# Performance work log

Measured on AMD Instinct MI355X. Metric: run time of the kernel, lower is better.

Reference implementation:

```python
import jax, jax.numpy as jnp
import numpy as np

N = 100000   # nodes
E = 1600000  # edges (avg degree 16)
IN, H, OUT = 64, 128, 1


def setup_inputs() -> dict:
    key = jax.random.key(0)
    ks = jax.random.split(key, 12)
    s = 0.05
    return {
        "x": jax.random.normal(ks[0], (N, IN), jnp.float32),
        "edge_index": jax.random.randint(ks[1], (2, E), 0, N, dtype=jnp.int64),
        "Wl1": jax.random.normal(ks[2], (IN, H), jnp.float32) * s,
        "Wr1": jax.random.normal(ks[3], (IN, H), jnp.float32) * s,
        "b1": jnp.zeros((H,), jnp.float32),
        "ln_g": jnp.ones((H,), jnp.float32),
        "ln_b": jnp.zeros((H,), jnp.float32),
        "Wres": jax.random.normal(ks[4], (IN, H), jnp.float32) * s,
        "bres": jnp.zeros((H,), jnp.float32),
        "Wl2": jax.random.normal(ks[5], (H, H), jnp.float32) * s,
        "Wr2": jax.random.normal(ks[6], (H, H), jnp.float32) * s,
        "b2": jnp.zeros((H,), jnp.float32),
        "Wl3": jax.random.normal(ks[7], (H, H), jnp.float32) * s,
        "Wr3": jax.random.normal(ks[8], (H, H), jnp.float32) * s,
        "b3": jnp.zeros((H,), jnp.float32),
        "Wl4": jax.random.normal(ks[9], (H, OUT), jnp.float32) * s,
        "Wr4": jax.random.normal(ks[10], (H, OUT), jnp.float32) * s,
        "b4": jnp.zeros((OUT,), jnp.float32),
    }


def _sage(h, src, dst, deg_inv, Wl, Wr, b):
    # PyG SAGEConv, aggr='mean': lin_l(mean_{j in N(i)} h_j) + lin_r(h_i)
    agg = jax.ops.segment_sum(h[src], dst, num_segments=N) * deg_inv[:, None]
    return agg @ Wl + h @ Wr + b


def _layernorm(h, g, b, eps=1e-5):
    mu = jnp.mean(h, axis=-1, keepdims=True)
    var = jnp.mean((h - mu) ** 2, axis=-1, keepdims=True)
    return (h - mu) * jax.lax.rsqrt(var + eps) * g + b


def reference(x, edge_index, Wl1, Wr1, b1, ln_g, ln_b, Wres, bres,
              Wl2, Wr2, b2, Wl3, Wr3, b3, Wl4, Wr4, b4):
    src, dst = edge_index[0], edge_index[1]
    deg = jax.ops.segment_sum(jnp.ones((E,), jnp.float32), dst, num_segments=N)
    deg_inv = 1.0 / jnp.maximum(deg, 1.0)

    h = jax.nn.relu(_layernorm(_sage(x, src, dst, deg_inv, Wl1, Wr1, b1), ln_g, ln_b))
    h = h + x @ Wres + bres              # residual (in_channel != hidden_channel)
    h = jax.nn.relu(_sage(h, src, dst, deg_inv, Wl2, Wr2, b2))   # dropout: eval no-op
    h = jax.nn.relu(_sage(h, src, dst, deg_inv, Wl3, Wr3, b3))
    out = _sage(h, src, dst, deg_inv, Wl4, Wr4, b4)
    return out.squeeze(-1)
```

## Files before the change

kernel.cpp:

```cpp
#include <hip/hip_runtime.h>
#include <hip/hip_bf16.h>

#define N_NODES 100000
#define N_EDGES 1600000

#define NBKT 782
#define SCAT_BLOCKS 240
#define BKT_CHUNK 6667

#define SORT_BLOCKS 40
#define SORT_CHUNK 2500
#define BH2_N (NBKT * SCAT_BLOCKS)
#define BHB ((BH2_N + 1023) / 1024)
#define XBF_BLOCKS 6250

#define NSTRIPS 6250
#define GEMM_BLOCKS 782

typedef __attribute__((ext_vector_type(8))) short short8v;
typedef __attribute__((ext_vector_type(4))) float float4v;

__device__ __forceinline__ unsigned short f2bf(float f) {
    unsigned int u = __float_as_uint(f);
    u = (u + 0x7FFFu + ((u >> 16) & 1u)) >> 16;
    return (unsigned short)u;
}
__device__ __forceinline__ float bf2f(unsigned short b) {
    return __uint_as_float((unsigned int)b << 16);
}

typedef __attribute__((address_space(1))) const unsigned int gld_g_t;
typedef __attribute__((address_space(3))) unsigned int gld_l_t;
__device__ __forceinline__ void gld_lds16(const void* g, void* l) {
    __builtin_amdgcn_global_load_lds((gld_g_t*)g, (gld_l_t*)l, 16, 0, 0);
}

#define SWZ128(row, ksh) ((row) * 128 + ((ksh) ^ (((row) & 7) << 3)))
#define SWZ256(row, ksh) ((row) * 256 + ((ksh) ^ (((row) & 7) << 3)))

__global__ __launch_bounds__(256) void hist_xbf_kernel(const int* __restrict__ ei, int* __restrict__ bh2,
                                                       const float* __restrict__ x, unsigned short* __restrict__ xcat) {
    __shared__ int h[NBKT];
    int tid = threadIdx.x;
    if (blockIdx.x < SCAT_BLOCKS) {
        for (int i = tid; i < NBKT; i += 256) h[i] = 0;
        __syncthreads();
        int start = blockIdx.x * BKT_CHUNK;
        int end = start + BKT_CHUNK; if (end > N_EDGES) end = N_EDGES;
        for (int i = start + tid; i < end; i += 256) {
            int d = ei[N_EDGES + i];
            atomicAdd(&h[d >> 7], 1);
        }
        __syncthreads();
        for (int i = tid; i < NBKT; i += 256) bh2[i * SCAT_BLOCKS + blockIdx.x] = h[i];
    } else {
        int idx = (blockIdx.x - SCAT_BLOCKS) * 256 + tid;
        if (idx < N_NODES * 16) {
            int node = idx >> 4;
            int f0 = (idx & 15) * 4;
            float4 v = *(const float4*)(x + (size_t)idx * 4);
            ushort4 o;
            o.x = f2bf(v.x); o.y = f2bf(v.y); o.z = f2bf(v.z); o.w = f2bf(v.w);
            *(ushort4*)(xcat + (size_t)node * 128 + f0) = o;
        }
    }
}

__global__ __launch_bounds__(256) void gscan_a_kernel(const int* __restrict__ in, int* __restrict__ bsum, int n) {
    __shared__ int lds[256];
    int tid = threadIdx.x;
    int base = blockIdx.x * 1024 + tid * 4;
    int s = 0;
    #pragma unroll
    for (int i = 0; i < 4; i++) s += (base + i < n) ? in[base + i] : 0;
    lds[tid] = s;
    __syncthreads();
    for (int off = 128; off; off >>= 1) {
        if (tid < off) lds[tid] += lds[tid + off];
        __syncthreads();
    }
    if (tid == 0) bsum[blockIdx.x] = lds[0];
}

__global__ __launch_bounds__(256) void gscan_c_kernel(int* __restrict__ data, const int* __restrict__ bsum,
                                                      int nb, int n) {
    __shared__ int sb[256];
    __shared__ int lds[256];
    int tid = threadIdx.x;
    sb[tid] = (tid < nb) ? bsum[tid] : 0;
    __syncthreads();
    for (int off = 1; off < 256; off <<= 1) {
        int y = 0;
        if (tid >= off) y = sb[tid - off];
        __syncthreads();
        if (tid >= off) sb[tid] += y;
        __syncthreads();
    }
    int blockbase = (blockIdx.x == 0) ? 0 : sb[blockIdx.x - 1];

    int base = blockIdx.x * 1024 + tid * 4;
    int v[4];
    int s = 0;
    #pragma unroll
    for (int i = 0; i < 4; i++) {
        v[i] = (base + i < n) ? data[base + i] : 0;
        s += v[i];
    }
    lds[tid] = s;
    __syncthreads();
    for (int off = 1; off < 256; off <<= 1) {
        int y = 0;
        if (tid >= off) y = lds[tid - off];
        __syncthreads();
        if (tid >= off) lds[tid] += y;
        __syncthreads();
    }
    int run = blockbase + lds[tid] - s;
    #pragma unroll
    for (int i = 0; i < 4; i++) {
        if (base + i < n) data[base + i] = run;
        run += v[i];
    }
}

__global__ __launch_bounds__(256) void bkt_scatter2_kernel(const int* __restrict__ ei, const int* __restrict__ bh2,
                                                           int* __restrict__ packed) {
    __shared__ int h[NBKT];
    __shared__ int base[NBKT];
    int tid = threadIdx.x;
    for (int i = tid; i < NBKT; i += 256) { h[i] = 0; base[i] = bh2[i * SCAT_BLOCKS + blockIdx.x]; }
    __syncthreads();
    int start = blockIdx.x * BKT_CHUNK;
    int end = start + BKT_CHUNK; if (end > N_EDGES) end = N_EDGES;
    for (int i = start + tid; i < end; i += 256) {
        int s = ei[i];
        int d = ei[N_EDGES + i];
        int b = d >> 7;
        int pos = base[b] + atomicAdd(&h[b], 1);
        packed[pos] = (s << 7) | (d & 127);
    }
}

__global__ __launch_bounds__(256) void bkt_build_kernel(const int* __restrict__ packed, const int* __restrict__ bh2,
                                                        int* __restrict__ deg, int* __restrict__ row_ptr,
                                                        int* __restrict__ col) {
    __shared__ int c[128];
    __shared__ int rp[128];
    int tid = threadIdx.x;
    int s0 = bh2[blockIdx.x * SCAT_BLOCKS];
    int s1 = (blockIdx.x + 1 < NBKT) ? bh2[(blockIdx.x + 1) * SCAT_BLOCKS] : N_EDGES;
    if (tid < 128) c[tid] = 0;
    __syncthreads();
    for (int i = s0 + tid; i < s1; i += 256) atomicAdd(&c[packed[i] & 127], 1);
    __syncthreads();
    if (tid < 128) rp[tid] = c[tid];
    __syncthreads();
    for (int off = 1; off < 128; off <<= 1) {
        int y = 0;
        if (tid >= off && tid < 128) y = rp[tid - off];
        __syncthreads();
        if (tid >= off && tid < 128) rp[tid] += y;
        __syncthreads();
    }
    int node = blockIdx.x * 128 + tid;
    if (tid < 128) {
        rp[tid] = s0 + rp[tid] - c[tid];
        if (node < N_NODES) {
            deg[node] = c[tid];
            row_ptr[node] = rp[tid];
        }
        c[tid] = 0;
    }
    if (blockIdx.x == 0 && tid == 0) row_ptr[N_NODES] = N_EDGES;
    __syncthreads();
    for (int i = s0 + tid; i < s1; i += 256) {
        int p = packed[i];
        int dl = p & 127;
        int pos = rp[dl] + atomicAdd(&c[dl], 1);
        col[pos] = p >> 7;
    }
}

__global__ __launch_bounds__(256) void dsort_hist_kernel(const int* __restrict__ deg, int* __restrict__ bh) {
    __shared__ int h[64];
    int tid = threadIdx.x;
    if (tid < 64) h[tid] = 0;
    __syncthreads();
    int start = blockIdx.x * SORT_CHUNK;
    int end = start + SORT_CHUNK; if (end > N_NODES) end = N_NODES;
    for (int i = start + tid; i < end; i += 256) atomicAdd(&h[min(deg[i], 63)], 1);
    __syncthreads();
    if (tid < 64) bh[tid * SORT_BLOCKS + blockIdx.x] = h[tid];
}

__global__ __launch_bounds__(256) void dsort_scat_kernel(const int* __restrict__ deg, const int* __restrict__ bh,
                                                         int* __restrict__ ord) {
    __shared__ int sbh[64 * SORT_BLOCKS];
    __shared__ int ps[256];
    __shared__ int h[64];
    int tid = threadIdx.x;
    int v[10];
    int s = 0;
    #pragma unroll
    for (int k = 0; k < 10; k++) { v[k] = bh[tid * 10 + k]; s += v[k]; }
    ps[tid] = s;
    if (tid < 64) h[tid] = 0;
    __syncthreads();
    for (int off = 1; off < 256; off <<= 1) {
        int y = 0;
        if (tid >= off) y = ps[tid - off];
        __syncthreads();
        if (tid >= off) ps[tid] += y;
        __syncthreads();
    }
    int run = ps[tid] - s;
    #pragma unroll
    for (int k = 0; k < 10; k++) { sbh[tid * 10 + k] = run; run += v[k]; }
    __syncthreads();
    int start = blockIdx.x * SORT_CHUNK;
    int end = start + SORT_CHUNK; if (end > N_NODES) end = N_NODES;
    for (int i = start + tid; i < end; i += 256) {
        int b = min(deg[i], 63);
        int pos = sbh[b * SORT_BLOCKS + blockIdx.x] + atomicAdd(&h[b], 1);
        ord[pos] = i;
    }
}

#define ACC4(u) { a0 += bf2f(u.x); a1 += bf2f(u.y); a2 += bf2f(u.z); a3 += bf2f(u.w); }

__global__ __launch_bounds__(256) void agg64_kernel(unsigned short* __restrict__ xcat,
                                                    const int* __restrict__ row_ptr, const int* __restrict__ col,
                                                    const int* __restrict__ ord) {
    int tid = threadIdx.x;
    int slot = blockIdx.x * 16 + (tid >> 4);
    if (slot >= N_NODES) return;
    int i = ord[slot];
    int f0 = (tid & 15) * 4;
    int s = row_ptr[i], e = row_ptr[i + 1];
    float a0 = 0.f, a1 = 0.f, a2 = 0.f, a3 = 0.f;
    int t = s;
    while (t + 7 < e) {
        int j0 = col[t], j1 = col[t + 1], j2 = col[t + 2], j3 = col[t + 3];
        int j4 = col[t + 4], j5 = col[t + 5], j6 = col[t + 6], j7 = col[t + 7];
        ushort4 u0 = *(const ushort4*)(xcat + (size_t)j0 * 128 + f0);
        ushort4 u1 = *(const ushort4*)(xcat + (size_t)j1 * 128 + f0);
        ushort4 u2 = *(const ushort4*)(xcat + (size_t)j2 * 128 + f0);
        ushort4 u3 = *(const ushort4*)(xcat + (size_t)j3 * 128 + f0);
        ushort4 u4 = *(const ushort4*)(xcat + (size_t)j4 * 128 + f0);
        ushort4 u5 = *(const ushort4*)(xcat + (size_t)j5 * 128 + f0);
        ushort4 u6 = *(const ushort4*)(xcat + (size_t)j6 * 128 + f0);
        ushort4 u7 = *(const ushort4*)(xcat + (size_t)j7 * 128 + f0);
        ACC4(u0) ACC4(u1) ACC4(u2) ACC4(u3) ACC4(u4) ACC4(u5) ACC4(u6) ACC4(u7)
        t += 8;
    }
    if (t + 3 < e) {
        int j0 = col[t], j1 = col[t + 1], j2 = col[t + 2], j3 = col[t + 3];
        ushort4 u0 = *(const ushort4*)(xcat + (size_t)j0 * 128 + f0);
        ushort4 u1 = *(const ushort4*)(xcat + (size_t)j1 * 128 + f0);
        ushort4 u2 = *(const ushort4*)(xcat + (size_t)j2 * 128 + f0);
        ushort4 u3 = *(const ushort4*)(xcat + (size_t)j3 * 128 + f0);
        ACC4(u0) ACC4(u1) ACC4(u2) ACC4(u3)
        t += 4;
    }
    if (t + 1 < e) {
        int j0 = col[t], j1 = col[t + 1];
        ushort4 u0 = *(const ushort4*)(xcat + (size_t)j0 * 128 + f0);
        ushort4 u1 = *(const ushort4*)(xcat + (size_t)j1 * 128 + f0);
        ACC4(u0) ACC4(u1)
        t += 2;
    }
    if (t < e) {
        ushort4 u0 = *(const ushort4*)(xcat + (size_t)col[t] * 128 + f0);
        ACC4(u0)
    }
    float di = 1.0f / fmaxf((float)(e - s), 1.0f);
    ushort4 o;
    o.x = f2bf(a0 * di); o.y = f2bf(a1 * di); o.z = f2bf(a2 * di); o.w = f2bf(a3 * di);
    *(ushort4*)(xcat + (size_t)i * 128 + 64 + f0) = o;
}

__global__ __launch_bounds__(256) void agg128_kernel(unsigned short* __restrict__ hcat,
                                                     const int* __restrict__ row_ptr, const int* __restrict__ col,
                                                     const int* __restrict__ ord) {
    int tid = threadIdx.x;
    int slot = blockIdx.x * 8 + (tid >> 5);
    if (slot >= N_NODES) return;
    int i = ord[slot];
    int f0 = (tid & 31) * 4;
    int s = row_ptr[i], e = row_ptr[i + 1];
    float a0 = 0.f, a1 = 0.f, a2 = 0.f, a3 = 0.f;
    int t = s;
    while (t + 7 < e) {
        int j0 = col[t], j1 = col[t + 1], j2 = col[t + 2], j3 = col[t + 3];
        int j4 = col[t + 4], j5 = col[t + 5], j6 = col[t + 6], j7 = col[t + 7];
        ushort4 u0 = *(const ushort4*)(hcat + (size_t)j0 * 256 + f0);
        ushort4 u1 = *(const ushort4*)(hcat + (size_t)j1 * 256 + f0);
        ushort4 u2 = *(const ushort4*)(hcat + (size_t)j2 * 256 + f0);
        ushort4 u3 = *(const ushort4*)(hcat + (size_t)j3 * 256 + f0);
        ushort4 u4 = *(const ushort4*)(hcat + (size_t)j4 * 256 + f0);
        ushort4 u5 = *(const ushort4*)(hcat + (size_t)j5 * 256 + f0);
        ushort4 u6 = *(const ushort4*)(hcat + (size_t)j6 * 256 + f0);
        ushort4 u7 = *(const ushort4*)(hcat + (size_t)j7 * 256 + f0);
        ACC4(u0) ACC4(u1) ACC4(u2) ACC4(u3) ACC4(u4) ACC4(u5) ACC4(u6) ACC4(u7)
        t += 8;
    }
    if (t + 3 < e) {
        int j0 = col[t], j1 = col[t + 1], j2 = col[t + 2], j3 = col[t + 3];
        ushort4 u0 = *(const ushort4*)(hcat + (size_t)j0 * 256 + f0);
        ushort4 u1 = *(const ushort4*)(hcat + (size_t)j1 * 256 + f0);
        ushort4 u2 = *(const ushort4*)(hcat + (size_t)j2 * 256 + f0);
        ushort4 u3 = *(const ushort4*)(hcat + (size_t)j3 * 256 + f0);
        ACC4(u0) ACC4(u1) ACC4(u2) ACC4(u3)
        t += 4;
    }
    if (t + 1 < e) {
        int j0 = col[t], j1 = col[t + 1];
        ushort4 u0 = *(const ushort4*)(hcat + (size_t)j0 * 256 + f0);
        ushort4 u1 = *(const ushort4*)(hcat + (size_t)j1 * 256 + f0);
        ACC4(u0) ACC4(u1)
        t += 2;
    }
    if (t < e) {
        ushort4 u0 = *(const ushort4*)(hcat + (size_t)col[t] * 256 + f0);
        ACC4(u0)
    }
    float di = 1.0f / fmaxf((float)(e - s), 1.0f);
    ushort4 o;
    o.x = f2bf(a0 * di); o.y = f2bf(a1 * di); o.z = f2bf(a2 * di); o.w = f2bf(a3 * di);
    *(ushort4*)(hcat + (size_t)i * 256 + 128 + f0) = o;
}

__global__ __launch_bounds__(256) void wprep_all_kernel(const float* __restrict__ Wr1, const float* __restrict__ Wl1,
                                                        const float* __restrict__ Wres,
                                                        const float* __restrict__ Wl2, const float* __restrict__ Wr2,
                                                        const float* __restrict__ Wl3, const float* __restrict__ Wr3,
                                                        unsigned short* __restrict__ Bt1,
                                                        unsigned short* __restrict__ Bt2,
                                                        unsigned short* __restrict__ Bt3) {
    int idx = blockIdx.x * 256 + threadIdx.x;
    int seg = idx >> 15;
    int loc = idx & 32767;
    if (seg == 0) {
        int n = loc >> 7;
        int k = loc & 127;
        float v;
        if (n < 128) v = (k < 64) ? Wr1[k * 128 + n] : Wl1[(k - 64) * 128 + n];
        else         v = (k < 64) ? Wres[k * 128 + (n - 128)] : 0.f;
        Bt1[loc] = f2bf(v);
    } else if (seg == 1) {
        int n = loc >> 8;
        int k = loc & 255;
        float v = (k < 128) ? Wr2[k * 128 + n] : Wl2[(k - 128) * 128 + n];
        Bt2[loc] = f2bf(v);
    } else if (seg == 2) {
        int n = loc >> 8;
        int k = loc & 255;
        float v = (k < 128) ? Wr3[k * 128 + n] : Wl3[(k - 128) * 128 + n];
        Bt3[loc] = f2bf(v);
    }
}

__global__ __launch_bounds__(512) void mgemm1_ln_kernel(const unsigned short* __restrict__ A,
                                                        const unsigned short* __restrict__ Bt,
                                                        const float* __restrict__ b1, const float* __restrict__ ln_g,
                                                        const float* __restrict__ ln_b, const float* __restrict__ bres,
                                                        unsigned short* __restrict__ hcat) {
    __shared__ unsigned short Bs[32768];
    int tid = threadIdx.x;
    int wave = tid >> 6, lane = tid & 63;
    int lm = lane & 15, lk = (lane >> 4) * 8;

    #pragma unroll
    for (int rnd = 0; rnd < 8; rnd++) {
        int Lb = rnd * 8192 + tid * 16;
        int row = Lb >> 8;
        int sb = (Lb & 255) ^ ((row & 7) << 4);
        gld_lds16(Bt + (size_t)row * 128 + (sb >> 1), &Bs[Lb >> 1]);
    }
    __syncthreads();

    int strip = blockIdx.x * 8 + wave;
    if (strip >= NSTRIPS) return;
    int m0 = strip * 16;

    float4v accT[8], accR[8];
    #pragma unroll
    for (int j = 0; j < 8; j++) { accT[j] = (float4v)0.f; accR[j] = (float4v)0.f; }

    const unsigned short* arow = A + (size_t)(m0 + lm) * 128 + lk;
    #pragma unroll
    for (int k0 = 0; k0 < 128; k0 += 32) {
        short8v af = *(const short8v*)(arow + k0);
        short8v bf[8];
        #pragma unroll
        for (int j = 0; j < 8; j++)
            bf[j] = *(const short8v*)&Bs[SWZ128(j * 16 + lm, k0 + lk)];
        #pragma unroll
        for (int j = 0; j < 8; j++)
            accT[j] = __builtin_amdgcn_mfma_f32_16x16x32_bf16(af, bf[j], accT[j], 0, 0, 0);
        if (k0 < 64) {
            short8v bg[8];
            #pragma unroll
            for (int j = 0; j < 8; j++)
                bg[j] = *(const short8v*)&Bs[SWZ128(128 + j * 16 + lm, k0 + lk)];
            #pragma unroll
            for (int j = 0; j < 8; j++)
                accR[j] = __builtin_amdgcn_mfma_f32_16x16x32_bf16(af, bg[j], accR[j], 0, 0, 0);
        }
    }

    float b1v[8], gv[8], bbv[8], brv[8];
    #pragma unroll
    for (int j = 0; j < 8; j++) {
        int cc = j * 16 + lm;
        b1v[j] = b1[cc]; gv[j] = ln_g[cc]; bbv[j] = ln_b[cc]; brv[j] = bres[cc];
    }
    int q4 = lane >> 4;
    #pragma unroll
    for (int r = 0; r < 4; r++) {
        float sp = 0.f, sq = 0.f;
        #pragma unroll
        for (int j = 0; j < 8; j++) {
            float tv = accT[j][r] + b1v[j];
            sp += tv; sq += tv * tv;
        }
        #pragma unroll
        for (int off = 1; off < 16; off <<= 1) {
            sp += __shfl_xor(sp, off);
            sq += __shfl_xor(sq, off);
        }
        float mu = sp * (1.f / 128.f);
        float var = sq * (1.f / 128.f) - mu * mu;
        float rstd = rsqrtf(var + 1e-5f);
        int gm = m0 + q4 * 4 + r;
        #pragma unroll
        for (int j = 0; j < 8; j++) {
            float tv = accT[j][r] + b1v[j];
            float y = fmaxf((tv - mu) * rstd * gv[j] + bbv[j], 0.f) + accR[j][r] + brv[j];
            hcat[(size_t)gm * 256 + j * 16 + lm] = f2bf(y);
        }
    }
}

__global__ __launch_bounds__(512) void mgemm_kernel(const unsigned short* __restrict__ A,
                                                    const unsigned short* __restrict__ Bt,
                                                    const float* __restrict__ bias,
                                                    unsigned short* __restrict__ C) {
    __shared__ unsigned short Bs[32768];
    int tid = threadIdx.x;
    int wave = tid >> 6, lane = tid & 63;
    int lm = lane & 15, lk = (lane >> 4) * 8;

    #pragma unroll
    for (int rnd = 0; rnd < 8; rnd++) {
        int Lb = rnd * 8192 + tid * 16;
        int row = Lb >> 9;
        int sb = (Lb & 511) ^ ((row & 7) << 4);
        gld_lds16(Bt + ((size_t)row << 8) + (sb >> 1), &Bs[Lb >> 1]);
    }
    __syncthreads();

    int strip = blockIdx.x * 8 + wave;
    if (strip >= NSTRIPS) return;
    int m0 = strip * 16;

    float4v acc[8];
    #pragma unroll
    for (int j = 0; j < 8; j++) acc[j] = (float4v)0.f;

    const unsigned short* arow = A + (size_t)(m0 + lm) * 256 + lk;
    #pragma unroll
    for (int k0 = 0; k0 < 256; k0 += 32) {
        short8v af = *(const short8v*)(arow + k0);
        short8v bf[8];
        #pragma unroll
        for (int j = 0; j < 8; j++)
            bf[j] = *(const short8v*)&Bs[SWZ256(j * 16 + lm, k0 + lk)];
        #pragma unroll
        for (int j = 0; j < 8; j++)
            acc[j] = __builtin_amdgcn_mfma_f32_16x16x32_bf16(af, bf[j], acc[j], 0, 0, 0);
    }

    int q4 = lane >> 4;
    #pragma unroll
    for (int j = 0; j < 8; j++) {
        int cc = j * 16 + lm;
        float bv = bias[cc];
        #pragma unroll
        for (int r = 0; r < 4; r++) {
            int m = m0 + q4 * 4 + r;
            C[(size_t)m * 256 + cc] = f2bf(fmaxf(acc[j][r] + bv, 0.f));
        }
    }
}

__global__ __launch_bounds__(512) void mgemm_pq_kernel(const unsigned short* __restrict__ A,
                                                       const unsigned short* __restrict__ Bt,
                                                       const float* __restrict__ bias,
                                                       const float* __restrict__ Wl4, const float* __restrict__ Wr4,
                                                       const float* __restrict__ b4,
                                                       float* __restrict__ p, float* __restrict__ q) {
    __shared__ unsigned short Bs[32768];
    int tid = threadIdx.x;
    int wave = tid >> 6, lane = tid & 63;
    int lm = lane & 15, lk = (lane >> 4) * 8;

    #pragma unroll
    for (int rnd = 0; rnd < 8; rnd++) {
        int Lb = rnd * 8192 + tid * 16;
        int row = Lb >> 9;
        int sb = (Lb & 511) ^ ((row & 7) << 4);
        gld_lds16(Bt + ((size_t)row << 8) + (sb >> 1), &Bs[Lb >> 1]);
    }
    __syncthreads();

    int strip = blockIdx.x * 8 + wave;
    if (strip >= NSTRIPS) return;
    int m0 = strip * 16;

    float4v acc[8];
    #pragma unroll
    for (int j = 0; j < 8; j++) acc[j] = (float4v)0.f;

    const unsigned short* arow = A + (size_t)(m0 + lm) * 256 + lk;
    #pragma unroll
    for (int k0 = 0; k0 < 256; k0 += 32) {
        short8v af = *(const short8v*)(arow + k0);
        short8v bf[8];
        #pragma unroll
        for (int j = 0; j < 8; j++)
            bf[j] = *(const short8v*)&Bs[SWZ256(j * 16 + lm, k0 + lk)];
        #pragma unroll
        for (int j = 0; j < 8; j++)
            acc[j] = __builtin_amdgcn_mfma_f32_16x16x32_bf16(af, bf[j], acc[j], 0, 0, 0);
    }

    float b3v[8], wlv[8], wrv[8];
    #pragma unroll
    for (int j = 0; j < 8; j++) {
        int cc = j * 16 + lm;
        b3v[j] = bias[cc]; wlv[j] = Wl4[cc]; wrv[j] = Wr4[cc];
    }
    float b4v = b4[0];
    int q4 = lane >> 4;
    #pragma unroll
    for (int r = 0; r < 4; r++) {
        float pp = 0.f, qq = 0.f;
        #pragma unroll
        for (int j = 0; j < 8; j++) {
            float hv = fmaxf(acc[j][r] + b3v[j], 0.f);
            pp += hv * wlv[j]; qq += hv * wrv[j];
        }
        #pragma unroll
        for (int off = 1; off < 16; off <<= 1) {
            pp += __shfl_xor(pp, off);
            qq += __shfl_xor(qq, off);
        }
        if (lm == 0) {
            int m = m0 + q4 * 4 + r;
            p[m] = pp;
            q[m] = qq + b4v;
        }
    }
}

__global__ __launch_bounds__(256) void final_kernel(const float* __restrict__ p, const float* __restrict__ q,
                                                    const int* __restrict__ row_ptr, const int* __restrict__ col,
                                                    float* __restrict__ out) {
    int i = blockIdx.x * 256 + threadIdx.x;
    if (i >= N_NODES) return;
    int s = row_ptr[i], e = row_ptr[i + 1];
    float acc = 0.f;
    int t = s;
    for (; t + 3 < e; t += 4)
        acc += p[col[t]] + p[col[t + 1]] + p[col[t + 2]] + p[col[t + 3]];
    for (; t < e; t++) acc += p[col[t]];
    float di = 1.0f / fmaxf((float)(e - s), 1.0f);
    out[i] = acc * di + q[i];
}


extern "C" void kernel_launch(void* const* d_in, const int* in_sizes, int n_in,
                              void* d_out, int out_size, void* d_ws, size_t ws_size,
                              hipStream_t stream) {
    const float* x    = (const float*)d_in[0];
    const int*   ei   = (const int*)d_in[1];
    const float* Wl1  = (const float*)d_in[2];
    const float* Wr1  = (const float*)d_in[3];
    const float* b1   = (const float*)d_in[4];
    const float* ln_g = (const float*)d_in[5];
    const float* ln_b = (const float*)d_in[6];
    const float* Wres = (const float*)d_in[7];
    const float* bres = (const float*)d_in[8];
    const float* Wl2  = (const float*)d_in[9];
    const float* Wr2  = (const float*)d_in[10];
    const float* b2   = (const float*)d_in[11];
    const float* Wl3  = (const float*)d_in[12];
    const float* Wr3  = (const float*)d_in[13];
    const float* b3   = (const float*)d_in[14];
    const float* Wl4  = (const float*)d_in[15];
    const float* Wr4  = (const float*)d_in[16];
    const float* b4   = (const float*)d_in[17];
    float* out = (float*)d_out;

    char* w = (char*)d_ws;
    size_t off = 0;
    auto alloc = [&](size_t bytes) -> void* {
        off = (off + 255) & ~(size_t)255;
        void* pp = w + off;
        off += bytes;
        return pp;
    };

    int*   deg        = (int*)alloc(N_NODES * 4);
    int*   row_ptr    = (int*)alloc((N_NODES + 1) * 4);
    int*   bsum       = (int*)alloc(1024);
    int*   col        = (int*)alloc(N_EDGES * 4);
    int*   bh2        = (int*)alloc(BH2_N * 4);
    int*   bh         = (int*)alloc(64 * SORT_BLOCKS * 4);
    int*   ord        = (int*)alloc(N_NODES * 4);
    unsigned short* Bt1  = (unsigned short*)alloc(256 * 128 * 2);
    unsigned short* Bt2  = (unsigned short*)alloc(128 * 256 * 2);
    unsigned short* Bt3  = (unsigned short*)alloc(128 * 256 * 2);
    unsigned short* xcat = (unsigned short*)alloc((size_t)N_NODES * 128 * 2);
    unsigned short* hcat = (unsigned short*)alloc((size_t)N_NODES * 256 * 2);
    int*   packed  = (int*)alloc((size_t)N_EDGES * 4);
    float* p       = (float*)alloc(N_NODES * 4);
    float* q       = (float*)alloc(N_NODES * 4);
    (void)ws_size; (void)n_in; (void)in_sizes; (void)out_size;

    const int NB = (N_NODES + 255) / 256;

    wprep_all_kernel<<<384, 256, 0, stream>>>(Wr1, Wl1, Wres, Wl2, Wr2, Wl3, Wr3, Bt1, Bt2, Bt3);

    hist_xbf_kernel<<<SCAT_BLOCKS + XBF_BLOCKS, 256, 0, stream>>>(ei, bh2, x, xcat);
    gscan_a_kernel<<<BHB, 256, 0, stream>>>(bh2, bsum, BH2_N);
    gscan_c_kernel<<<BHB, 256, 0, stream>>>(bh2, bsum, BHB, BH2_N);
    bkt_scatter2_kernel<<<SCAT_BLOCKS, 256, 0, stream>>>(ei, bh2, packed);
    bkt_build_kernel<<<NBKT, 256, 0, stream>>>(packed, bh2, deg, row_ptr, col);
    dsort_hist_kernel<<<SORT_BLOCKS, 256, 0, stream>>>(deg, bh);
    dsort_scat_kernel<<<SORT_BLOCKS, 256, 0, stream>>>(deg, bh, ord);

    agg64_kernel<<<(N_NODES + 15) / 16, 256, 0, stream>>>(xcat, row_ptr, col, ord);
    mgemm1_ln_kernel<<<GEMM_BLOCKS, 512, 0, stream>>>(xcat, Bt1, b1, ln_g, ln_b, bres, hcat);

    agg128_kernel<<<(N_NODES + 7) / 8, 256, 0, stream>>>(hcat, row_ptr, col, ord);
    mgemm_kernel<<<GEMM_BLOCKS, 512, 0, stream>>>(hcat, Bt2, b2, hcat);

    agg128_kernel<<<(N_NODES + 7) / 8, 256, 0, stream>>>(hcat, row_ptr, col, ord);
    mgemm_pq_kernel<<<GEMM_BLOCKS, 512, 0, stream>>>(hcat, Bt3, b3, Wl4, Wr4, b4, p, q);

    final_kernel<<<NB, 256, 0, stream>>>(p, q, row_ptr, col, out);
}
```

Before: 372.9 us.

## Split concatenated feature buffers into separate source and aggregate arrays

Concatenated [self | aggregated] bf16 rows are replaced by separate dense source and aggregate arrays. Neighbour gathers then read from a compact table with half the row stride, which shrinks the gathered working set and should improve cache reuse. The GEMMs now read their A operand from two pointers, choosing one per k-step. It also reverses the degree-sort order so high-degree nodes are scheduled first, and unrolls the final scalar gather by 8; the cost is slightly more pointer arithmetic in the GEMM A loads.

```diff
diff --git a/kernel.cpp b/kernel.cpp
--- a/kernel.cpp
+++ b/kernel.cpp
@@ -39,7 +39,7 @@
 #define SWZ256(row, ksh) ((row) * 256 + ((ksh) ^ (((row) & 7) << 3)))
 
 __global__ __launch_bounds__(256) void hist_xbf_kernel(const int* __restrict__ ei, int* __restrict__ bh2,
-                                                       const float* __restrict__ x, unsigned short* __restrict__ xcat) {
+                                                       const float* __restrict__ x, unsigned short* __restrict__ xsrc) {
     __shared__ int h[NBKT];
     int tid = threadIdx.x;
     if (blockIdx.x < SCAT_BLOCKS) {
@@ -61,7 +61,7 @@
             float4 v = *(const float4*)(x + (size_t)idx * 4);
             ushort4 o;
             o.x = f2bf(v.x); o.y = f2bf(v.y); o.z = f2bf(v.z); o.w = f2bf(v.w);
-            *(ushort4*)(xcat + (size_t)node * 128 + f0) = o;
+            *(ushort4*)(xsrc + (size_t)node * 64 + f0) = o;
         }
     }
 }
@@ -188,7 +188,7 @@
     __syncthreads();
     int start = blockIdx.x * SORT_CHUNK;
     int end = start + SORT_CHUNK; if (end > N_NODES) end = N_NODES;
-    for (int i = start + tid; i < end; i += 256) atomicAdd(&h[min(deg[i], 63)], 1);
+    for (int i = start + tid; i < end; i += 256) atomicAdd(&h[63 - min(deg[i], 63)], 1);
     __syncthreads();
     if (tid < 64) bh[tid * SORT_BLOCKS + blockIdx.x] = h[tid];
 }
@@ -220,7 +220,7 @@
     int start = blockIdx.x * SORT_CHUNK;
     int end = start + SORT_CHUNK; if (end > N_NODES) end = N_NODES;
     for (int i = start + tid; i < end; i += 256) {
-        int b = min(deg[i], 63);
+        int b = 63 - min(deg[i], 63);
         int pos = sbh[b * SORT_BLOCKS + blockIdx.x] + atomicAdd(&h[b], 1);
         ord[pos] = i;
     }
@@ -228,7 +228,8 @@
 
 #define ACC4(u) { a0 += bf2f(u.x); a1 += bf2f(u.y); a2 += bf2f(u.z); a3 += bf2f(u.w); }
 
-__global__ __launch_bounds__(256) void agg64_kernel(unsigned short* __restrict__ xcat,
+__global__ __launch_bounds__(256) void agg64_kernel(const unsigned short* __restrict__ xsrc,
+                                                    unsigned short* __restrict__ aggx,
                                                     const int* __restrict__ row_ptr, const int* __restrict__ col,
                                                     const int* __restrict__ ord) {
     int tid = threadIdx.x;
@@ -242,44 +243,45 @@
     while (t + 7 < e) {
         int j0 = col[t], j1 = col[t + 1], j2 = col[t + 2], j3 = col[t + 3];
         int j4 = col[t + 4], j5 = col[t + 5], j6 = col[t + 6], j7 = col[t + 7];
-        ushort4 u0 = *(const ushort4*)(xcat + (size_t)j0 * 128 + f0);
-        ushort4 u1 = *(const ushort4*)(xcat + (size_t)j1 * 128 + f0);
-        ushort4 u2 = *(const ushort4*)(xcat + (size_t)j2 * 128 + f0);
-        ushort4 u3 = *(const ushort4*)(xcat + (size_t)j3 * 128 + f0);
-        ushort4 u4 = *(const ushort4*)(xcat + (size_t)j4 * 128 + f0);
-        ushort4 u5 = *(const ushort4*)(xcat + (size_t)j5 * 128 + f0);
-        ushort4 u6 = *(const ushort4*)(xcat + (size_t)j6 * 128 + f0);
-        ushort4 u7 = *(const ushort4*)(xcat + (size_t)j7 * 128 + f0);
+        ushort4 u0 = *(const ushort4*)(xsrc + (size_t)j0 * 64 + f0);
+        ushort4 u1 = *(const ushort4*)(xsrc + (size_t)j1 * 64 + f0);
+        ushort4 u2 = *(const ushort4*)(xsrc + (size_t)j2 * 64 + f0);
+        ushort4 u3 = *(const ushort4*)(xsrc + (size_t)j3 * 64 + f0);
+        ushort4 u4 = *(const ushort4*)(xsrc + (size_t)j4 * 64 + f0);
+        ushort4 u5 = *(const ushort4*)(xsrc + (size_t)j5 * 64 + f0);
+        ushort4 u6 = *(const ushort4*)(xsrc + (size_t)j6 * 64 + f0);
+        ushort4 u7 = *(const ushort4*)(xsrc + (size_t)j7 * 64 + f0);
         ACC4(u0) ACC4(u1) ACC4(u2) ACC4(u3) ACC4(u4) ACC4(u5) ACC4(u6) ACC4(u7)
         t += 8;
     }
     if (t + 3 < e) {
         int j0 = col[t], j1 = col[t + 1], j2 = col[t + 2], j3 = col[t + 3];
-        ushort4 u0 = *(const ushort4*)(xcat + (size_t)j0 * 128 + f0);
-        ushort4 u1 = *(const ushort4*)(xcat + (size_t)j1 * 128 + f0);
-        ushort4 u2 = *(const ushort4*)(xcat + (size_t)j2 * 128 + f0);
-        ushort4 u3 = *(const ushort4*)(xcat + (size_t)j3 * 128 + f0);
+        ushort4 u0 = *(const ushort4*)(xsrc + (size_t)j0 * 64 + f0);
+        ushort4 u1 = *(const ushort4*)(xsrc + (size_t)j1 * 64 + f0);
+        ushort4 u2 = *(const ushort4*)(xsrc + (size_t)j2 * 64 + f0);
+        ushort4 u3 = *(const ushort4*)(xsrc + (size_t)j3 * 64 + f0);
         ACC4(u0) ACC4(u1) ACC4(u2) ACC4(u3)
         t += 4;
     }
     if (t + 1 < e) {
         int j0 = col[t], j1 = col[t + 1];
-        ushort4 u0 = *(const ushort4*)(xcat + (size_t)j0 * 128 + f0);
-        ushort4 u1 = *(const ushort4*)(xcat + (size_t)j1 * 128 + f0);
+        ushort4 u0 = *(const ushort4*)(xsrc + (size_t)j0 * 64 + f0);
+        ushort4 u1 = *(const ushort4*)(xsrc + (size_t)j1 * 64 + f0);
         ACC4(u0) ACC4(u1)
         t += 2;
     }
     if (t < e) {
-        ushort4 u0 = *(const ushort4*)(xcat + (size_t)col[t] * 128 + f0);
+        ushort4 u0 = *(const ushort4*)(xsrc + (size_t)col[t] * 64 + f0);
         ACC4(u0)
     }
     float di = 1.0f / fmaxf((float)(e - s), 1.0f);
     ushort4 o;
     o.x = f2bf(a0 * di); o.y = f2bf(a1 * di); o.z = f2bf(a2 * di); o.w = f2bf(a3 * di);
-    *(ushort4*)(xcat + (size_t)i * 128 + 64 + f0) = o;
-}
-
-__global__ __launch_bounds__(256) void agg128_kernel(unsigned short* __restrict__ hcat,
+    *(ushort4*)(aggx + (size_t)i * 64 + f0) = o;
+}
+
+__global__ __launch_bounds__(256) void agg128_kernel(const unsigned short* __restrict__ hsrc,
+                                                     unsigned short* __restrict__ aggh,
                                                      const int* __restrict__ row_ptr, const int* __restrict__ col,
                                                      const int* __restrict__ ord) {
     int tid = threadIdx.x;
@@ -293,41 +295,41 @@
     while (t + 7 < e) {
         int j0 = col[t], j1 = col[t + 1], j2 = col[t + 2], j3 = col[t + 3];
         int j4 = col[t + 4], j5 = col[t + 5], j6 = col[t + 6], j7 = col[t + 7];
-        ushort4 u0 = *(const ushort4*)(hcat + (size_t)j0 * 256 + f0);
-        ushort4 u1 = *(const ushort4*)(hcat + (size_t)j1 * 256 + f0);
-        ushort4 u2 = *(const ushort4*)(hcat + (size_t)j2 * 256 + f0);
-        ushort4 u3 = *(const ushort4*)(hcat + (size_t)j3 * 256 + f0);
-        ushort4 u4 = *(const ushort4*)(hcat + (size_t)j4 * 256 + f0);
-        ushort4 u5 = *(const ushort4*)(hcat + (size_t)j5 * 256 + f0);
-        ushort4 u6 = *(const ushort4*)(hcat + (size_t)j6 * 256 + f0);
-        ushort4 u7 = *(const ushort4*)(hcat + (size_t)j7 * 256 + f0);
+        ushort4 u0 = *(const ushort4*)(hsrc + (size_t)j0 * 128 + f0);
+        ushort4 u1 = *(const ushort4*)(hsrc + (size_t)j1 * 128 + f0);
+        ushort4 u2 = *(const ushort4*)(hsrc + (size_t)j2 * 128 + f0);
+        ushort4 u3 = *(const ushort4*)(hsrc + (size_t)j3 * 128 + f0);
+        ushort4 u4 = *(const ushort4*)(hsrc + (size_t)j4 * 128 + f0);
+        ushort4 u5 = *(const ushort4*)(hsrc + (size_t)j5 * 128 + f0);
+        ushort4 u6 = *(const ushort4*)(hsrc + (size_t)j6 * 128 + f0);
+        ushort4 u7 = *(const ushort4*)(hsrc + (size_t)j7 * 128 + f0);
         ACC4(u0) ACC4(u1) ACC4(u2) ACC4(u3) ACC4(u4) ACC4(u5) ACC4(u6) ACC4(u7)
         t += 8;
     }
     if (t + 3 < e) {
         int j0 = col[t], j1 = col[t + 1], j2 = col[t + 2], j3 = col[t + 3];
-        ushort4 u0 = *(const ushort4*)(hcat + (size_t)j0 * 256 + f0);
-        ushort4 u1 = *(const ushort4*)(hcat + (size_t)j1 * 256 + f0);
-        ushort4 u2 = *(const ushort4*)(hcat + (size_t)j2 * 256 + f0);
-        ushort4 u3 = *(const ushort4*)(hcat + (size_t)j3 * 256 + f0);
+        ushort4 u0 = *(const ushort4*)(hsrc + (size_t)j0 * 128 + f0);
+        ushort4 u1 = *(const ushort4*)(hsrc + (size_t)j1 * 128 + f0);
+        ushort4 u2 = *(const ushort4*)(hsrc + (size_t)j2 * 128 + f0);
+        ushort4 u3 = *(const ushort4*)(hsrc + (size_t)j3 * 128 + f0);
         ACC4(u0) ACC4(u1) ACC4(u2) ACC4(u3)
         t += 4;
     }
     if (t + 1 < e) {
         int j0 = col[t], j1 = col[t + 1];
-        ushort4 u0 = *(const ushort4*)(hcat + (size_t)j0 * 256 + f0);
-        ushort4 u1 = *(const ushort4*)(hcat + (size_t)j1 * 256 + f0);
+        ushort4 u0 = *(const ushort4*)(hsrc + (size_t)j0 * 128 + f0);
+        ushort4 u1 = *(const ushort4*)(hsrc + (size_t)j1 * 128 + f0);
         ACC4(u0) ACC4(u1)
         t += 2;
     }
     if (t < e) {
-        ushort4 u0 = *(const ushort4*)(hcat + (size_t)col[t] * 256 + f0);
+        ushort4 u0 = *(const ushort4*)(hsrc + (size_t)col[t] * 128 + f0);
         ACC4(u0)
     }
     float di = 1.0f / fmaxf((float)(e - s), 1.0f);
     ushort4 o;
     o.x = f2bf(a0 * di); o.y = f2bf(a1 * di); o.z = f2bf(a2 * di); o.w = f2bf(a3 * di);
-    *(ushort4*)(hcat + (size_t)i * 256 + 128 + f0) = o;
+    *(ushort4*)(aggh + (size_t)i * 128 + f0) = o;
 }
 
 __global__ __launch_bounds__(256) void wprep_all_kernel(const float* __restrict__ Wr1, const float* __restrict__ Wl1,
@@ -360,11 +362,12 @@
     }
 }
 
-__global__ __launch_bounds__(512) void mgemm1_ln_kernel(const unsigned short* __restrict__ A,
+__global__ __launch_bounds__(512) void mgemm1_ln_kernel(const unsigned short* __restrict__ Ax,
+                                                        const unsigned short* __restrict__ Aa,
                                                         const unsigned short* __restrict__ Bt,
                                                         const float* __restrict__ b1, const float* __restrict__ ln_g,
                                                         const float* __restrict__ ln_b, const float* __restrict__ bres,
-                                                        unsigned short* __restrict__ hcat) {
+                                                        unsigned short* __restrict__ hsrc) {
     __shared__ unsigned short Bs[32768];
     int tid = threadIdx.x;
     int wave = tid >> 6, lane = tid & 63;
@@ -387,10 +390,11 @@
     #pragma unroll
     for (int j = 0; j < 8; j++) { accT[j] = (float4v)0.f; accR[j] = (float4v)0.f; }
 
-    const unsigned short* arow = A + (size_t)(m0 + lm) * 128 + lk;
+    const unsigned short* arx = Ax + (size_t)(m0 + lm) * 64 + lk;
+    const unsigned short* ara = Aa + (size_t)(m0 + lm) * 64 + lk;
     #pragma unroll
     for (int k0 = 0; k0 < 128; k0 += 32) {
-        short8v af = *(const short8v*)(arow + k0);
+        short8v af = (k0 < 64) ? *(const short8v*)(arx + k0) : *(const short8v*)(ara + (k0 - 64));
         short8v bf[8];
         #pragma unroll
         for (int j = 0; j < 8; j++)
@@ -437,12 +441,13 @@
         for (int j = 0; j < 8; j++) {
             float tv = accT[j][r] + b1v[j];
             float y = fmaxf((tv - mu) * rstd * gv[j] + bbv[j], 0.f) + accR[j][r] + brv[j];
-            hcat[(size_t)gm * 256 + j * 16 + lm] = f2bf(y);
-        }
-    }
-}
-
-__global__ __launch_bounds__(512) void mgemm_kernel(const unsigned short* __restrict__ A,
+            hsrc[(size_t)gm * 128 + j * 16 + lm] = f2bf(y);
+        }
+    }
+}
+
+__global__ __launch_bounds__(512) void mgemm_kernel(const unsigned short* __restrict__ Ah,
+                                                    const unsigned short* __restrict__ Aa,
                                                     const unsigned short* __restrict__ Bt,
                                                     const float* __restrict__ bias,
                                                     unsigned short* __restrict__ C) {
@@ -468,10 +473,11 @@
     #pragma unroll
     for (int j = 0; j < 8; j++) acc[j] = (float4v)0.f;
 
-    const unsigned short* arow = A + (size_t)(m0 + lm) * 256 + lk;
+    const unsigned short* arh = Ah + (size_t)(m0 + lm) * 128 + lk;
+    const unsigned short* ara = Aa + (size_t)(m0 + lm) * 128 + lk;
     #pragma unroll
     for (int k0 = 0; k0 < 256; k0 += 32) {
-        short8v af = *(const short8v*)(arow + k0);
+        short8v af = (k0 < 128) ? *(const short8v*)(arh + k0) : *(const short8v*)(ara + (k0 - 128));
         short8v bf[8];
         #pragma unroll
         for (int j = 0; j < 8; j++)
@@ -489,12 +495,13 @@
         #pragma unroll
         for (int r = 0; r < 4; r++) {
             int m = m0 + q4 * 4 + r;
-            C[(size_t)m * 256 + cc] = f2bf(fmaxf(acc[j][r] + bv, 0.f));
-        }
-    }
-}
-
-__global__ __launch_bounds__(512) void mgemm_pq_kernel(const unsigned short* __restrict__ A,
+            C[(size_t)m * 128 + cc] = f2bf(fmaxf(acc[j][r] + bv, 0.f));
+        }
+    }
+}
+
+__global__ __launch_bounds__(512) void mgemm_pq_kernel(const unsigned short* __restrict__ Ah,
+                                                       const unsigned short* __restrict__ Aa,
                                                        const unsigned short* __restrict__ Bt,
                                                        const float* __restrict__ bias,
                                                        const float* __restrict__ Wl4, const float* __restrict__ Wr4,
@@ -522,10 +529,11 @@
     #pragma unroll
     for (int j = 0; j < 8; j++) acc[j] = (float4v)0.f;
 
-    const unsigned short* arow = A + (size_t)(m0 + lm) * 256 + lk;
+    const unsigned short* arh = Ah + (size_t)(m0 + lm) * 128 + lk;
+    const unsigned short* ara = Aa + (size_t)(m0 + lm) * 128 + lk;
     #pragma unroll
     for (int k0 = 0; k0 < 256; k0 += 32) {
-        short8v af = *(const short8v*)(arow + k0);
+        short8v af = (k0 < 128) ? *(const short8v*)(arh + k0) : *(const short8v*)(ara + (k0 - 128));
         short8v bf[8];
         #pragma unroll
         for (int j = 0; j < 8; j++)
@@ -572,8 +580,9 @@
     int s = row_ptr[i], e = row_ptr[i + 1];
     float acc = 0.f;
     int t = s;
-    for (; t + 3 < e; t += 4)
-        acc += p[col[t]] + p[col[t + 1]] + p[col[t + 2]] + p[col[t + 3]];
+    for (; t + 7 < e; t += 8)
+        acc += p[col[t]] + p[col[t + 1]] + p[col[t + 2]] + p[col[t + 3]]
+             + p[col[t + 4]] + p[col[t + 5]] + p[col[t + 6]] + p[col[t + 7]];
     for (; t < e; t++) acc += p[col[t]];
     float di = 1.0f / fmaxf((float)(e - s), 1.0f);
     out[i] = acc * di + q[i];
@@ -622,8 +631,10 @@
     unsigned short* Bt1  = (unsigned short*)alloc(256 * 128 * 2);
     unsigned short* Bt2  = (unsigned short*)alloc(128 * 256 * 2);
     unsigned short* Bt3  = (unsigned short*)alloc(128 * 256 * 2);
-    unsigned short* xcat = (unsigned short*)alloc((size_t)N_NODES * 128 * 2);
-    unsigned short* hcat = (unsigned short*)alloc((size_t)N_NODES * 256 * 2);
+    unsigned short* xsrc = (unsigned short*)alloc((size_t)N_NODES * 64 * 2);
+    unsigned short* aggx = (unsigned short*)alloc((size_t)N_NODES * 64 * 2);
+    unsigned short* hsrc = (unsigned short*)alloc((size_t)N_NODES * 128 * 2);
+    unsigned short* aggh = (unsigned short*)alloc((size_t)N_NODES * 128 * 2);
     int*   packed  = (int*)alloc((size_t)N_EDGES * 4);
     float* p       = (float*)alloc(N_NODES * 4);
     float* q       = (float*)alloc(N_NODES * 4);
@@ -633,7 +644,7 @@
 
     wprep_all_kernel<<<384, 256, 0, stream>>>(Wr1, Wl1, Wres, Wl2, Wr2, Wl3, Wr3, Bt1, Bt2, Bt3);
 
-    hist_xbf_kernel<<<SCAT_BLOCKS + XBF_BLOCKS, 256, 0, stream>>>(ei, bh2, x, xcat);
+    hist_xbf_kernel<<<SCAT_BLOCKS + XBF_BLOCKS, 256, 0, stream>>>(ei, bh2, x, xsrc);
     gscan_a_kernel<<<BHB, 256, 0, stream>>>(bh2, bsum, BH2_N);
     gscan_c_kernel<<<BHB, 256, 0, stream>>>(bh2, bsum, BHB, BH2_N);
     bkt_scatter2_kernel<<<SCAT_BLOCKS, 256, 0, stream>>>(ei, bh2, packed);
@@ -641,14 +652,14 @@
     dsort_hist_kernel<<<SORT_BLOCKS, 256, 0, stream>>>(deg, bh);
     dsort_scat_kernel<<<SORT_BLOCKS, 256, 0, stream>>>(deg, bh, ord);
 
-    agg64_kernel<<<(N_NODES + 15) / 16, 256, 0, stream>>>(xcat, row_ptr, col, ord);
-    mgemm1_ln_kernel<<<GEMM_BLOCKS, 512, 0, stream>>>(xcat, Bt1, b1, ln_g, ln_b, bres, hcat);
-
-    agg128_kernel<<<(N_NODES + 7) / 8, 256, 0, stream>>>(hcat, row_ptr, col, ord);
-    mgemm_kernel<<<GEMM_BLOCKS, 512, 0, stream>>>(hcat, Bt2, b2, hcat);
-
-    agg128_kernel<<<(N_NODES + 7) / 8, 256, 0, stream>>>(hcat, row_ptr, col, ord);
-    mgemm_pq_kernel<<<GEMM_BLOCKS, 512, 0, stream>>>(hcat, Bt3, b3, Wl4, Wr4, b4, p, q);
+    agg64_kernel<<<(N_NODES + 15) / 16, 256, 0, stream>>>(xsrc, aggx, row_ptr, col, ord);
+    mgemm1_ln_kernel<<<GEMM_BLOCKS, 512, 0, stream>>>(xsrc, aggx, Bt1, b1, ln_g, ln_b, bres, hsrc);
+
+    agg128_kernel<<<(N_NODES + 7) / 8, 256, 0, stream>>>(hsrc, aggh, row_ptr, col, ord);
+    mgemm_kernel<<<GEMM_BLOCKS, 512, 0, stream>>>(hsrc, aggh, Bt2, b2, hsrc);
+
+    agg128_kernel<<<(N_NODES + 7) / 8, 256, 0, stream>>>(hsrc, aggh, row_ptr, col, ord);
+    mgemm_pq_kernel<<<GEMM_BLOCKS, 512, 0, stream>>>(hsrc, aggh, Bt3, b3, Wl4, Wr4, b4, p, q);
 
     final_kernel<<<NB, 256, 0, stream>>>(p, q, row_ptr, col, out);
 }
```

Result: no change. 368.2 us (-1.3%).
